# Kernel tuning notes

Measured on AMD Instinct MI355X. Metric: run time of the kernel, lower is better.

## Reference

```python
import jax, jax.numpy as jnp
import numpy as np

N = 100000
IN_F = 165
HID = 128
E = 1600000


def gcn_conv(x, W, b, src, dst, n):
    # PyG GCNConv: h = x @ W; add self-loops; symmetric norm D^-1/2 A D^-1/2; aggregate; + bias
    h = x @ W  # [n, out]
    src_sl = jnp.concatenate([src, jnp.arange(n)])
    dst_sl = jnp.concatenate([dst, jnp.arange(n)])
    deg = jax.ops.segment_sum(jnp.ones_like(src_sl, dtype=h.dtype), dst_sl, num_segments=n)
    dinv = jnp.where(deg > 0, jax.lax.rsqrt(deg), 0.0)
    norm = dinv[src_sl] * dinv[dst_sl]  # [e+n]
    msg = h[src_sl] * norm[:, None]
    out = jax.ops.segment_sum(msg, dst_sl, num_segments=n)
    return out + b


def setup_inputs() -> dict:
    key = jax.random.key(0)
    k = jax.random.split(key, 8)
    x = jax.random.normal(k[0], (N, IN_F), dtype=jnp.float32)
    edge_index = jax.random.randint(k[1], (2, E), 0, N)
    s1 = 1.0 / np.sqrt(IN_F)
    s2 = 1.0 / np.sqrt(HID)
    W1 = jax.random.uniform(k[2], (IN_F, HID), jnp.float32, -s1, s1)
    b1 = jnp.zeros((HID,), jnp.float32)
    W2 = jax.random.uniform(k[3], (HID, HID), jnp.float32, -s2, s2)
    b2 = jnp.zeros((HID,), jnp.float32)
    Wc = jax.random.uniform(k[4], (HID, 2), jnp.float32, -s2, s2)
    bc = jax.random.uniform(k[5], (2,), jnp.float32, -s2, s2)
    return {"x": x, "edge_index": edge_index, "W1": W1, "b1": b1,
            "W2": W2, "b2": b2, "Wc": Wc, "bc": bc}


def reference(x, edge_index, W1, b1, W2, b2, Wc, bc):
    src, dst = edge_index[0], edge_index[1]
    h = jax.nn.relu(gcn_conv(x, W1, b1, src, dst, N))
    # dropout inactive (eval mode)
    h = jax.nn.relu(gcn_conv(h, W2, b2, src, dst, N))
    return h @ Wc + bc
```

## Files before the change

kernel.cpp:

```cpp
#include <hip/hip_runtime.h>


typedef _Float16 half8 __attribute__((ext_vector_type(8)));
typedef float floatx4 __attribute__((ext_vector_type(4)));
typedef float f4u __attribute__((ext_vector_type(4), aligned(4)));

#define SLOT_C 64
#define BCAP 4608
#define NBKT 391
#define CHUNK 4096

__global__ __launch_bounds__(256) void multisplit_k(const int* __restrict__ src,
                                                    const int* __restrict__ dst, int e,
                                                    int* __restrict__ bcnt,
                                                    int2* __restrict__ edges2) {
  __shared__ int lhist[NBKT];
  __shared__ int lbase[NBKT];
  __shared__ int lcur[NBKT];
  int t = threadIdx.x;
  int e0 = blockIdx.x * CHUNK;
  int e1 = min(e0 + CHUNK, e);
  for (int b = t; b < NBKT; b += 256) { lhist[b] = 0; lcur[b] = 0; }
  __syncthreads();
  for (int i = e0 + t; i < e1; i += 256)
    atomicAdd(&lhist[dst[i] >> 8], 1);
  __syncthreads();
  for (int b = t; b < NBKT; b += 256) {
    int h = lhist[b];
    lbase[b] = h ? atomicAdd(&bcnt[b], h) : 0;
  }
  __syncthreads();
  for (int i = e0 + t; i < e1; i += 256) {
    int d = dst[i];
    int b = d >> 8;
    int p = lbase[b] + atomicAdd(&lcur[b], 1);
    if (p < BCAP) edges2[(size_t)b * BCAP + p] = make_int2(src[i], d);
  }
}

__global__ __launch_bounds__(256) void csr_from_bins_k(const int2* __restrict__ edges2,
                                                       const int* __restrict__ bcnt,
                                                       int* __restrict__ csr,
                                                       float* __restrict__ dinv, int n) {
  __shared__ int lcnt[256];
  int b = blockIdx.x;
  int node0 = b << 8;
  int t = threadIdx.x;
  lcnt[t] = 0;
  __syncthreads();
  int ec = min(bcnt[b], BCAP);
  const int2* ebase = edges2 + (size_t)b * BCAP;
  for (int i = t; i < ec; i += 256) {
    int2 ed = ebase[i];
    int p = atomicAdd(&lcnt[ed.y - node0], 1);
    if (p < SLOT_C - 1) csr[((size_t)ed.y << 6) + p] = ed.x;
  }
  __syncthreads();
  int node = node0 + t;
  if (node < n) {
    int c = lcnt[t];
    csr[((size_t)node << 6) + (SLOT_C - 1)] = c;
    dinv[node] = rsqrtf((float)(c + 1));
  }
}

__global__ void w_split_frag_k(const float* __restrict__ W, int K, int nslab,
                               _Float16* __restrict__ WF) {
  int idx = blockIdx.x * blockDim.x + threadIdx.x;
  if (idx >= nslab * 8192) return;
  int j = idx & 7;
  int lane = (idx >> 3) & 63;
  int p = (idx >> 9) & 1;
  int c = (idx >> 10) & 7;
  int s = idx >> 13;
  int k = (s << 5) + ((lane >> 4) << 3) + j;
  int col = (c << 4) + (lane & 15);
  float v = (k < K) ? W[(size_t)k * 128 + col] : 0.f;
  _Float16 h = (_Float16)v;
  WF[idx] = p ? (_Float16)(v - (float)h) : h;
}

template <bool AHALF, int NSLAB>
__global__ __launch_bounds__(256) void gemm_f16_k(const void* __restrict__ Av,
                                                  const _Float16* __restrict__ WF,
                                                  const float* __restrict__ rowscale,
                                                  _Float16* __restrict__ out,
                                                  int n, int K) {
  int wave = threadIdx.x >> 6, lane = threadIdx.x & 63;
  int m = lane & 15, quad = lane >> 4;
  int rowbase = blockIdx.x * 128 + wave * 32;
  int ra[2];
  ra[0] = min(rowbase + m, n - 1);
  ra[1] = min(rowbase + 16 + m, n - 1);

  floatx4 acc[2][8];
#pragma unroll
  for (int t = 0; t < 2; ++t)
#pragma unroll
    for (int c = 0; c < 8; ++c) acc[t][c] = (floatx4){0.f, 0.f, 0.f, 0.f};

  f4u xb[3][2][2];
  half8 hb[3][2];

  auto loadA = [&](int s, int b) {
    int k0 = (s << 5) + quad * 8;
#pragma unroll
    for (int t = 0; t < 2; ++t) {
      if constexpr (AHALF) {
        const _Float16* arow = (const _Float16*)Av + (size_t)ra[t] * K;
        hb[b][t] = *(const half8*)(arow + k0);
      } else {
        const float* arow = (const float*)Av + (size_t)ra[t] * K;
        if ((s << 5) + 32 <= K) {
          xb[b][t][0] = *(const f4u*)(arow + k0);
          xb[b][t][1] = *(const f4u*)(arow + k0 + 4);
        } else {
#pragma unroll
          for (int j = 0; j < 4; ++j) { int kk = k0 + j;     kk = kk < K ? kk : K - 1; xb[b][t][0][j] = arow[kk]; }
#pragma unroll
          for (int j = 0; j < 4; ++j) { int kk = k0 + 4 + j; kk = kk < K ? kk : K - 1; xb[b][t][1][j] = arow[kk]; }
        }
      }
    }
  };

  loadA(0, 0);
  if (NSLAB > 1) loadA(1, 1);

#pragma unroll
  for (int s = 0; s < NSLAB; ++s) {
    const _Float16* wbase = WF + (size_t)s * 8192;
    half8 wh[8], wl[8];
#pragma unroll
    for (int c = 0; c < 8; ++c) {
      wh[c] = *(const half8*)(wbase + c * 1024 + lane * 8);
      wl[c] = *(const half8*)(wbase + c * 1024 + 512 + lane * 8);
    }
    if (s + 2 < NSLAB) loadA(s + 2, (s + 2) % 3);

    int b = s % 3;
    half8 ah[2], al[2];
#pragma unroll
    for (int t = 0; t < 2; ++t) {
      if constexpr (AHALF) {
        ah[t] = hb[b][t];
      } else {
#pragma unroll
        for (int j = 0; j < 8; ++j) {
          float v = (j < 4) ? xb[b][t][0][j] : xb[b][t][1][j - 4];
          _Float16 hh = (_Float16)v;
          ah[t][j] = hh;
          al[t][j] = (_Float16)(v - (float)hh);
        }
      }
    }
#pragma unroll
    for (int c = 0; c < 8; ++c)
#pragma unroll
      for (int t = 0; t < 2; ++t) {
        acc[t][c] = __builtin_amdgcn_mfma_f32_16x16x32_f16(ah[t], wh[c], acc[t][c], 0, 0, 0);
        acc[t][c] = __builtin_amdgcn_mfma_f32_16x16x32_f16(ah[t], wl[c], acc[t][c], 0, 0, 0);
        if constexpr (!AHALF)
          acc[t][c] = __builtin_amdgcn_mfma_f32_16x16x32_f16(al[t], wh[c], acc[t][c], 0, 0, 0);
      }
  }

#pragma unroll
  for (int t = 0; t < 2; ++t) {
#pragma unroll
    for (int i = 0; i < 4; ++i) {
      int row = rowbase + t * 16 + quad * 4 + i;
      if (row < n) {
        float di = rowscale ? rowscale[row] : 1.0f;
#pragma unroll
        for (int c = 0; c < 8; ++c)
          out[(size_t)row * 128 + c * 16 + m] = (_Float16)(acc[t][c][i] * di);
      }
    }
  }
}

template <bool CLS>
__global__ __launch_bounds__(256) void aggregate_k(const _Float16* __restrict__ g,
                                                   const int* __restrict__ csr,
                                                   const float* __restrict__ dinv,
                                                   const float* __restrict__ bias,
                                                   const float* __restrict__ Wc,
                                                   const float* __restrict__ bc,
                                                   _Float16* __restrict__ out16,
                                                   float* __restrict__ out32, int n) {
  int wave = threadIdx.x >> 6;
  int lane = threadIdx.x & 63;
  int i = blockIdx.x * 4 + wave;
  if (i >= n) return;
  int qtr = lane >> 4;
  int l16 = lane & 15;
  int f = l16 * 8;

  int sv = csr[((size_t)i << 6) + lane];
  half8 self = *(const half8*)&g[(size_t)i * 128 + f];
  float di = dinv[i];
  float4 b0 = *(const float4*)&bias[f];
  float4 b1 = *(const float4*)&bias[f + 4];

  int deg = min(__shfl(sv, SLOT_C - 1, 64), SLOT_C - 1);

  float acc[8];
#pragma unroll
  for (int j = 0; j < 8; ++j) acc[j] = 0.f;

  auto grp = [&](int k) {
    int ee = 4 * k + qtr;
    bool valid = ee < deg;
    int ec = valid ? ee : 0;
    int srow = __shfl(sv, ec, 64);
    half8 v = *(const half8*)&g[(size_t)srow * 128 + f];
    float w = valid ? 1.f : 0.f;
#pragma unroll
    for (int j = 0; j < 8; ++j) acc[j] = fmaf(w, (float)v[j], acc[j]);
  };

  if (deg > 0) {
    if (deg <= 16) {
#pragma unroll
      for (int k = 0; k < 4; ++k) grp(k);
    } else if (deg <= 32) {
#pragma unroll
      for (int k = 0; k < 8; ++k) grp(k);
    } else {
#pragma unroll
      for (int k = 0; k < 16; ++k) grp(k);
    }
#pragma unroll
    for (int j = 0; j < 8; ++j) {
      acc[j] += __shfl_xor(acc[j], 16, 64);
      acc[j] += __shfl_xor(acc[j], 32, 64);
    }
  }

  float bv[8] = {b0.x, b0.y, b0.z, b0.w, b1.x, b1.y, b1.z, b1.w};
  float r[8];
#pragma unroll
  for (int j = 0; j < 8; ++j)
    r[j] = fmaxf((acc[j] + (float)self[j]) * di + bv[j], 0.f);

  if (!CLS) {
    if (qtr == 0) {
      half8 o;
#pragma unroll
      for (int j = 0; j < 8; ++j) o[j] = (_Float16)(r[j] * di);
      *(half8*)&out16[(size_t)i * 128 + f] = o;
    }
  } else {
    float c0v = 0.f, c1v = 0.f;
#pragma unroll
    for (int q = 0; q < 4; ++q) {
      float4 wv = *(const float4*)&Wc[f * 2 + q * 4];
      c0v += r[q * 2] * wv.x + r[q * 2 + 1] * wv.z;
      c1v += r[q * 2] * wv.y + r[q * 2 + 1] * wv.w;
    }
#pragma unroll
    for (int off = 8; off > 0; off >>= 1) {
      c0v += __shfl_down(c0v, off, 16);
      c1v += __shfl_down(c1v, off, 16);
    }
    if (lane == 0) {
      out32[(size_t)i * 2 + 0] = c0v + bc[0];
      out32[(size_t)i * 2 + 1] = c1v + bc[1];
    }
  }
}

extern "C" void kernel_launch(void* const* d_in, const int* in_sizes, int n_in,
                              void* d_out, int out_size, void* d_ws, size_t ws_size,
                              hipStream_t stream) {
  const float* x  = (const float*)d_in[0];
  const int*   ei = (const int*)d_in[1];
  const float* W1 = (const float*)d_in[2];
  const float* b1 = (const float*)d_in[3];
  const float* W2 = (const float*)d_in[4];
  const float* b2 = (const float*)d_in[5];
  const float* Wc = (const float*)d_in[6];
  const float* bc = (const float*)d_in[7];
  float* out = (float*)d_out;

  const int IN_F = 165;
  const int NS1 = 6;
  const int NS2 = 4;
  const int n = in_sizes[0] / IN_F;
  const int e = in_sizes[1] / 2;
  const int* src = ei;
  const int* dst = ei + e;

  char* ws = (char*)d_ws;
  size_t off = 0;
  auto alloc = [&](size_t bytes) -> void* {
    void* p = ws + off;
    off += (bytes + 255) & ~(size_t)255;
    return p;
  };
  _Float16* bufA = (_Float16*)alloc((size_t)n * 128 * 2);
  _Float16* bufB = (_Float16*)alloc((size_t)n * 128 * 2);
  int*   csr  = (int*)alloc((size_t)n * SLOT_C * 4);
  int2*  edges2 = (int2*)alloc((size_t)NBKT * BCAP * 8);
  int*   bcnt = (int*)alloc((size_t)NBKT * 4);
  float* dinv = (float*)alloc((size_t)n * 4);
  _Float16* wf1 = (_Float16*)alloc((size_t)NS1 * 8192 * 2);
  _Float16* wf2 = (_Float16*)alloc((size_t)NS2 * 8192 * 2);

  hipMemsetAsync(bcnt, 0, (size_t)NBKT * 4, stream);

  w_split_frag_k<<<NS1 * 32, 256, 0, stream>>>(W1, IN_F, NS1, wf1);
  w_split_frag_k<<<NS2 * 32, 256, 0, stream>>>(W2, 128, NS2, wf2);

  multisplit_k<<<(e + CHUNK - 1) / CHUNK, 256, 0, stream>>>(src, dst, e, bcnt, edges2);
  csr_from_bins_k<<<NBKT, 256, 0, stream>>>(edges2, bcnt, csr, dinv, n);

  const int gemmgrid = (n + 127) / 128;
  gemm_f16_k<false, NS1><<<gemmgrid, 256, 0, stream>>>(x, wf1, dinv, bufA, n, IN_F);
  aggregate_k<false><<<(n + 3) / 4, 256, 0, stream>>>(bufA, csr, dinv, b1, nullptr, nullptr,
                                                      bufB, nullptr, n);
  gemm_f16_k<true, NS2><<<gemmgrid, 256, 0, stream>>>(bufB, wf2, nullptr, bufA, n, 128);
  aggregate_k<true><<<(n + 3) / 4, 256, 0, stream>>>(bufA, csr, dinv, b2, Wc, bc,
                                                     nullptr, out, n);
}
```

Baseline: 342.2 us.

## Split feature matrix and CSR into halves for cache-friendly aggregation

Splits the 128-wide fp16 hidden feature buffers into two 64-column halves. Each aggregation block handles one half for four nodes, with blocks interleaved so both halves of a node group run close together, and each wave covers 8 edges per step instead of 4. This shrinks the gathered working set per pass, so the half-size feature table is more likely to stay in L2/LLC during random gathers. The CSR is split into a 31-entry primary slab plus an overflow slab, so low-degree nodes read less index data. The classifier output now takes two atomic adds per node into a zeroed output, which adds a memset, doubles the number of blocks, and needs extra shuffles.

```diff
diff --git a/kernel.cpp b/kernel.cpp
--- a/kernel.cpp
+++ b/kernel.cpp
@@ -40,7 +40,8 @@
 
 __global__ __launch_bounds__(256) void csr_from_bins_k(const int2* __restrict__ edges2,
                                                        const int* __restrict__ bcnt,
-                                                       int* __restrict__ csr,
+                                                       int* __restrict__ csrA,
+                                                       int* __restrict__ csrB,
                                                        float* __restrict__ dinv, int n) {
   __shared__ int lcnt[256];
   int b = blockIdx.x;
@@ -53,13 +54,14 @@
   for (int i = t; i < ec; i += 256) {
     int2 ed = ebase[i];
     int p = atomicAdd(&lcnt[ed.y - node0], 1);
-    if (p < SLOT_C - 1) csr[((size_t)ed.y << 6) + p] = ed.x;
+    if (p < 31) csrA[((size_t)ed.y << 5) + p] = ed.x;
+    else if (p < SLOT_C - 1) csrB[((size_t)ed.y << 5) + (p - 31)] = ed.x;
   }
   __syncthreads();
   int node = node0 + t;
   if (node < n) {
     int c = lcnt[t];
-    csr[((size_t)node << 6) + (SLOT_C - 1)] = c;
+    csrA[((size_t)node << 5) + 31] = c;
     dinv[node] = rsqrtf((float)(c + 1));
   }
 }
@@ -81,10 +83,12 @@
 }
 
 template <bool AHALF, int NSLAB>
-__global__ __launch_bounds__(256) void gemm_f16_k(const void* __restrict__ Av,
+__global__ __launch_bounds__(256) void gemm_f16_k(const void* __restrict__ A0,
+                                                  const void* __restrict__ A1,
                                                   const _Float16* __restrict__ WF,
                                                   const float* __restrict__ rowscale,
-                                                  _Float16* __restrict__ out,
+                                                  _Float16* __restrict__ out0,
+                                                  _Float16* __restrict__ out1,
                                                   int n, int K) {
   int wave = threadIdx.x >> 6, lane = threadIdx.x & 63;
   int m = lane & 15, quad = lane >> 4;
@@ -107,10 +111,10 @@
 #pragma unroll
     for (int t = 0; t < 2; ++t) {
       if constexpr (AHALF) {
-        const _Float16* arow = (const _Float16*)Av + (size_t)ra[t] * K;
-        hb[b][t] = *(const half8*)(arow + k0);
+        const _Float16* base = (const _Float16*)(((s << 5) < 64) ? A0 : A1);
+        hb[b][t] = *(const half8*)(base + (size_t)ra[t] * 64 + (k0 & 63));
       } else {
-        const float* arow = (const float*)Av + (size_t)ra[t] * K;
+        const float* arow = (const float*)A0 + (size_t)ra[t] * K;
         if ((s << 5) + 32 <= K) {
           xb[b][t][0] = *(const f4u*)(arow + k0);
           xb[b][t][1] = *(const f4u*)(arow + k0 + 4);
@@ -173,48 +177,57 @@
       if (row < n) {
         float di = rowscale ? rowscale[row] : 1.0f;
 #pragma unroll
-        for (int c = 0; c < 8; ++c)
-          out[(size_t)row * 128 + c * 16 + m] = (_Float16)(acc[t][c][i] * di);
+        for (int c = 0; c < 8; ++c) {
+          _Float16* o = (c < 4) ? out0 : out1;
+          o[(size_t)row * 64 + (c & 3) * 16 + m] = (_Float16)(acc[t][c][i] * di);
+        }
       }
     }
   }
 }
 
 template <bool CLS>
-__global__ __launch_bounds__(256) void aggregate_k(const _Float16* __restrict__ g,
-                                                   const int* __restrict__ csr,
+__global__ __launch_bounds__(256) void aggregate_k(const _Float16* __restrict__ g0,
+                                                   const _Float16* __restrict__ g1,
+                                                   const int* __restrict__ csrA,
+                                                   const int* __restrict__ csrB,
                                                    const float* __restrict__ dinv,
                                                    const float* __restrict__ bias,
                                                    const float* __restrict__ Wc,
                                                    const float* __restrict__ bc,
-                                                   _Float16* __restrict__ out16,
+                                                   _Float16* __restrict__ o0,
+                                                   _Float16* __restrict__ o1,
                                                    float* __restrict__ out32, int n) {
   int wave = threadIdx.x >> 6;
   int lane = threadIdx.x & 63;
-  int i = blockIdx.x * 4 + wave;
+  int blk = blockIdx.x;
+  int h = (blk >> 2) & 1;
+  int ng = (blk >> 3) * 4 + (blk & 3);
+  int i = ng * 4 + wave;
   if (i >= n) return;
-  int qtr = lane >> 4;
-  int l16 = lane & 15;
-  int f = l16 * 8;
-
-  int sv = csr[((size_t)i << 6) + lane];
-  half8 self = *(const half8*)&g[(size_t)i * 128 + f];
+  int g8 = lane >> 3;
+  int f = (lane & 7) * 8;
+
+  const _Float16* g = h ? g1 : g0;
+
+  int sv = csrA[((size_t)i << 5) + (lane & 31)];
+  half8 self = *(const half8*)&g[(size_t)i * 64 + f];
   float di = dinv[i];
-  float4 b0 = *(const float4*)&bias[f];
-  float4 b1 = *(const float4*)&bias[f + 4];
-
-  int deg = min(__shfl(sv, SLOT_C - 1, 64), SLOT_C - 1);
+  float4 bv0 = *(const float4*)&bias[h * 64 + f];
+  float4 bv1 = *(const float4*)&bias[h * 64 + f + 4];
+
+  int deg = min(__shfl(sv, 31, 64), SLOT_C - 1);
 
   float acc[8];
 #pragma unroll
   for (int j = 0; j < 8; ++j) acc[j] = 0.f;
 
-  auto grp = [&](int k) {
-    int ee = 4 * k + qtr;
+  auto grpS = [&](int k) {
+    int ee = 8 * k + g8;
     bool valid = ee < deg;
     int ec = valid ? ee : 0;
     int srow = __shfl(sv, ec, 64);
-    half8 v = *(const half8*)&g[(size_t)srow * 128 + f];
+    half8 v = *(const half8*)&g[(size_t)srow * 64 + f];
     float w = valid ? 1.f : 0.f;
 #pragma unroll
     for (int j = 0; j < 8; ++j) acc[j] = fmaf(w, (float)v[j], acc[j]);
@@ -222,51 +235,63 @@
 
   if (deg > 0) {
     if (deg <= 16) {
-#pragma unroll
-      for (int k = 0; k < 4; ++k) grp(k);
-    } else if (deg <= 32) {
-#pragma unroll
-      for (int k = 0; k < 8; ++k) grp(k);
+      grpS(0); grpS(1);
+    } else if (deg <= 31) {
+#pragma unroll
+      for (int k = 0; k < 4; ++k) grpS(k);
     } else {
-#pragma unroll
-      for (int k = 0; k < 16; ++k) grp(k);
+      int sv2 = csrB[((size_t)i << 5) + (lane & 31)];
+#pragma unroll
+      for (int k = 0; k < 8; ++k) {
+        int ee = 8 * k + g8;
+        bool valid = ee < deg;
+        int ec = valid ? ee : 0;
+        int sA = __shfl(sv, ec < 31 ? ec : 0, 64);
+        int sB = __shfl(sv2, ec >= 31 ? ec - 31 : 0, 64);
+        int srow = (ec < 31) ? sA : sB;
+        half8 v = *(const half8*)&g[(size_t)srow * 64 + f];
+        float w = valid ? 1.f : 0.f;
+#pragma unroll
+        for (int j = 0; j < 8; ++j) acc[j] = fmaf(w, (float)v[j], acc[j]);
+      }
     }
 #pragma unroll
     for (int j = 0; j < 8; ++j) {
+      acc[j] += __shfl_xor(acc[j], 8, 64);
       acc[j] += __shfl_xor(acc[j], 16, 64);
       acc[j] += __shfl_xor(acc[j], 32, 64);
     }
   }
 
-  float bv[8] = {b0.x, b0.y, b0.z, b0.w, b1.x, b1.y, b1.z, b1.w};
+  float bv[8] = {bv0.x, bv0.y, bv0.z, bv0.w, bv1.x, bv1.y, bv1.z, bv1.w};
   float r[8];
 #pragma unroll
   for (int j = 0; j < 8; ++j)
     r[j] = fmaxf((acc[j] + (float)self[j]) * di + bv[j], 0.f);
 
   if (!CLS) {
-    if (qtr == 0) {
+    if (g8 == 0) {
       half8 o;
 #pragma unroll
       for (int j = 0; j < 8; ++j) o[j] = (_Float16)(r[j] * di);
-      *(half8*)&out16[(size_t)i * 128 + f] = o;
+      *(half8*)&((h ? o1 : o0)[(size_t)i * 64 + f]) = o;
     }
   } else {
     float c0v = 0.f, c1v = 0.f;
 #pragma unroll
     for (int q = 0; q < 4; ++q) {
-      float4 wv = *(const float4*)&Wc[f * 2 + q * 4];
+      float4 wv = *(const float4*)&Wc[(h * 64 + f) * 2 + q * 4];
       c0v += r[q * 2] * wv.x + r[q * 2 + 1] * wv.z;
       c1v += r[q * 2] * wv.y + r[q * 2 + 1] * wv.w;
     }
 #pragma unroll
-    for (int off = 8; off > 0; off >>= 1) {
-      c0v += __shfl_down(c0v, off, 16);
-      c1v += __shfl_down(c1v, off, 16);
+    for (int off = 4; off > 0; off >>= 1) {
+      c0v += __shfl_down(c0v, off, 8);
+      c1v += __shfl_down(c1v, off, 8);
     }
     if (lane == 0) {
-      out32[(size_t)i * 2 + 0] = c0v + bc[0];
-      out32[(size_t)i * 2 + 1] = c1v + bc[1];
+      atomicAdd(&out32[(size_t)i * 2 + 0], h == 0 ? c0v + bc[0] : c0v);
+      atomicAdd(&out32[(size_t)i * 2 + 1], h == 0 ? c1v + bc[1] : c1v);
     }
   }
 }
@@ -299,9 +324,12 @@
     off += (bytes + 255) & ~(size_t)255;
     return p;
   };
-  _Float16* bufA = (_Float16*)alloc((size_t)n * 128 * 2);
-  _Float16* bufB = (_Float16*)alloc((size_t)n * 128 * 2);
-  int*   csr  = (int*)alloc((size_t)n * SLOT_C * 4);
+  _Float16* bufA0 = (_Float16*)alloc((size_t)n * 64 * 2);
+  _Float16* bufA1 = (_Float16*)alloc((size_t)n * 64 * 2);
+  _Float16* bufB0 = (_Float16*)alloc((size_t)n * 64 * 2);
+  _Float16* bufB1 = (_Float16*)alloc((size_t)n * 64 * 2);
+  int*   csrA = (int*)alloc((size_t)n * 32 * 4);
+  int*   csrB = (int*)alloc((size_t)n * 32 * 4);
   int2*  edges2 = (int2*)alloc((size_t)NBKT * BCAP * 8);
   int*   bcnt = (int*)alloc((size_t)NBKT * 4);
   float* dinv = (float*)alloc((size_t)n * 4);
@@ -309,18 +337,24 @@
   _Float16* wf2 = (_Float16*)alloc((size_t)NS2 * 8192 * 2);
 
   hipMemsetAsync(bcnt, 0, (size_t)NBKT * 4, stream);
+  hipMemsetAsync(out, 0, (size_t)n * 2 * sizeof(float), stream);
 
   w_split_frag_k<<<NS1 * 32, 256, 0, stream>>>(W1, IN_F, NS1, wf1);
   w_split_frag_k<<<NS2 * 32, 256, 0, stream>>>(W2, 128, NS2, wf2);
 
   multisplit_k<<<(e + CHUNK - 1) / CHUNK, 256, 0, stream>>>(src, dst, e, bcnt, edges2);
-  csr_from_bins_k<<<NBKT, 256, 0, stream>>>(edges2, bcnt, csr, dinv, n);
+  csr_from_bins_k<<<NBKT, 256, 0, stream>>>(edges2, bcnt, csrA, csrB, dinv, n);
 
   const int gemmgrid = (n + 127) / 128;
-  gemm_f16_k<false, NS1><<<gemmgrid, 256, 0, stream>>>(x, wf1, dinv, bufA, n, IN_F);
-  aggregate_k<false><<<(n + 3) / 4, 256, 0, stream>>>(bufA, csr, dinv, b1, nullptr, nullptr,
-                                                      bufB, nullptr, n);
-  gemm_f16_k<true, NS2><<<gemmgrid, 256, 0, stream>>>(bufB, wf2, nullptr, bufA, n, 128);
-  aggregate_k<true><<<(n + 3) / 4, 256, 0, stream>>>(bufA, csr, dinv, b2, Wc, bc,
-                                                     nullptr, out, n);
-}
+  const int G = (n + 3) / 4;
+  const int Gp = (G + 3) & ~3;
+  const int agrid = 2 * Gp;
+  gemm_f16_k<false, NS1><<<gemmgrid, 256, 0, stream>>>(x, nullptr, wf1, dinv,
+                                                       bufA0, bufA1, n, IN_F);
+  aggregate_k<false><<<agrid, 256, 0, stream>>>(bufA0, bufA1, csrA, csrB, dinv, b1,
+                                                nullptr, nullptr, bufB0, bufB1, nullptr, n);
+  gemm_f16_k<true, NS2><<<gemmgrid, 256, 0, stream>>>(bufB0, bufB1, wf2, nullptr,
+                                                      bufA0, bufA1, n, 128);
+  aggregate_k<true><<<agrid, 256, 0, stream>>>(bufA0, bufA1, csrA, csrB, dinv, b2,
+                                               Wc, bc, nullptr, nullptr, out, n);
+}
```

Result: slower. 403.1 us (+17.8%).

## Replace global-atomic bucket binning with per-chunk local sort and offset table

Applied to the files above, without the earlier changes.

The edge binning step now sorts each 4096-edge chunk locally by destination bucket using a shared-memory histogram and wave prefix scan. It writes the chunk in place and records per-chunk bucket start offsets as ushort, instead of reserving slots in global buckets with atomics on a shared counter array. The CSR build kernel then walks every chunk's segment for its bucket using the offset table. This removes the global atomics, the fixed BCAP bucket capacity and its overflow truncation, and the memset. In exchange, each CSR block reads 391 small scattered segments, which gives poorly coalesced, short loops per chunk.

```diff
diff --git a/kernel.cpp b/kernel.cpp
--- a/kernel.cpp
+++ b/kernel.cpp
@@ -6,54 +6,95 @@
 typedef float f4u __attribute__((ext_vector_type(4), aligned(4)));
 
 #define SLOT_C 64
-#define BCAP 4608
 #define NBKT 391
 #define CHUNK 4096
-
-__global__ __launch_bounds__(256) void multisplit_k(const int* __restrict__ src,
+#define GSTRIDE (NBKT + 1)
+
+__global__ __launch_bounds__(256) void sort_chunk_k(const int* __restrict__ src,
                                                     const int* __restrict__ dst, int e,
-                                                    int* __restrict__ bcnt,
-                                                    int2* __restrict__ edges2) {
+                                                    int2* __restrict__ sorted,
+                                                    unsigned short* __restrict__ gstart) {
   __shared__ int lhist[NBKT];
-  __shared__ int lbase[NBKT];
+  __shared__ int lstart[NBKT];
   __shared__ int lcur[NBKT];
+  __shared__ int lsegtot[8];
   int t = threadIdx.x;
   int e0 = blockIdx.x * CHUNK;
   int e1 = min(e0 + CHUNK, e);
+  int cnt = e1 - e0;
   for (int b = t; b < NBKT; b += 256) { lhist[b] = 0; lcur[b] = 0; }
   __syncthreads();
   for (int i = e0 + t; i < e1; i += 256)
     atomicAdd(&lhist[dst[i] >> 8], 1);
   __syncthreads();
+  int wave = t >> 6, lane = t & 63;
+  for (int seg = wave; seg < 7; seg += 4) {
+    int b = seg * 64 + lane;
+    int v = (b < NBKT) ? lhist[b] : 0;
+#pragma unroll
+    for (int off = 1; off < 64; off <<= 1) {
+      int u = __shfl_up(v, off, 64);
+      if (lane >= off) v += u;
+    }
+    if (b < NBKT) lstart[b] = v;
+    if (lane == 63) lsegtot[seg] = v;
+  }
+  __syncthreads();
+  if (wave == 0) {
+    int v = (lane < 7) ? lsegtot[lane] : 0;
+#pragma unroll
+    for (int off = 1; off < 8; off <<= 1) {
+      int u = __shfl_up(v, off, 64);
+      if (lane >= off) v += u;
+    }
+    if (lane < 7) lsegtot[lane] = v;
+  }
+  __syncthreads();
   for (int b = t; b < NBKT; b += 256) {
-    int h = lhist[b];
-    lbase[b] = h ? atomicAdd(&bcnt[b], h) : 0;
-  }
+    int s = lstart[b] - lhist[b] + ((b >= 64) ? lsegtot[(b >> 6) - 1] : 0);
+    lstart[b] = s;
+    gstart[(size_t)blockIdx.x * GSTRIDE + b] = (unsigned short)s;
+  }
+  if (t == 0) gstart[(size_t)blockIdx.x * GSTRIDE + NBKT] = (unsigned short)cnt;
   __syncthreads();
   for (int i = e0 + t; i < e1; i += 256) {
     int d = dst[i];
     int b = d >> 8;
-    int p = lbase[b] + atomicAdd(&lcur[b], 1);
-    if (p < BCAP) edges2[(size_t)b * BCAP + p] = make_int2(src[i], d);
-  }
-}
-
-__global__ __launch_bounds__(256) void csr_from_bins_k(const int2* __restrict__ edges2,
-                                                       const int* __restrict__ bcnt,
-                                                       int* __restrict__ csr,
-                                                       float* __restrict__ dinv, int n) {
+    int p = lstart[b] + atomicAdd(&lcur[b], 1);
+    sorted[(size_t)blockIdx.x * CHUNK + p] = make_int2(src[i], d);
+  }
+}
+
+__global__ __launch_bounds__(256) void csr_from_sorted_k(const int2* __restrict__ sorted,
+                                                         const unsigned short* __restrict__ gstart,
+                                                         int nb, int* __restrict__ csr,
+                                                         float* __restrict__ dinv, int n) {
   __shared__ int lcnt[256];
   int b = blockIdx.x;
   int node0 = b << 8;
   int t = threadIdx.x;
   lcnt[t] = 0;
   __syncthreads();
-  int ec = min(bcnt[b], BCAP);
-  const int2* ebase = edges2 + (size_t)b * BCAP;
-  for (int i = t; i < ec; i += 256) {
-    int2 ed = ebase[i];
-    int p = atomicAdd(&lcnt[ed.y - node0], 1);
-    if (p < SLOT_C - 1) csr[((size_t)ed.y << 6) + p] = ed.x;
+  int Q = t >> 4;
+  int l16 = t & 15;
+  int s0 = 0, s1 = 0;
+  if (Q < nb) {
+    s0 = gstart[(size_t)Q * GSTRIDE + b];
+    s1 = gstart[(size_t)Q * GSTRIDE + b + 1];
+  }
+  for (int B = Q; B < nb; B += 16) {
+    int Bn = B + 16;
+    int n0 = 0, n1 = 0;
+    if (Bn < nb) {
+      n0 = gstart[(size_t)Bn * GSTRIDE + b];
+      n1 = gstart[(size_t)Bn * GSTRIDE + b + 1];
+    }
+    for (int jj = l16; jj < s1 - s0; jj += 16) {
+      int2 ed = sorted[(size_t)B * CHUNK + s0 + jj];
+      int p = atomicAdd(&lcnt[ed.y - node0], 1);
+      if (p < SLOT_C - 1) csr[((size_t)ed.y << 6) + p] = ed.x;
+    }
+    s0 = n0; s1 = n1;
   }
   __syncthreads();
   int node = node0 + t;
@@ -291,6 +332,7 @@
   const int e = in_sizes[1] / 2;
   const int* src = ei;
   const int* dst = ei + e;
+  const int NB = (e + CHUNK - 1) / CHUNK;
 
   char* ws = (char*)d_ws;
   size_t off = 0;
@@ -302,19 +344,17 @@
   _Float16* bufA = (_Float16*)alloc((size_t)n * 128 * 2);
   _Float16* bufB = (_Float16*)alloc((size_t)n * 128 * 2);
   int*   csr  = (int*)alloc((size_t)n * SLOT_C * 4);
-  int2*  edges2 = (int2*)alloc((size_t)NBKT * BCAP * 8);
-  int*   bcnt = (int*)alloc((size_t)NBKT * 4);
+  int2*  sorted = (int2*)alloc((size_t)NB * CHUNK * 8);
+  unsigned short* gstart = (unsigned short*)alloc((size_t)NB * GSTRIDE * 2);
   float* dinv = (float*)alloc((size_t)n * 4);
   _Float16* wf1 = (_Float16*)alloc((size_t)NS1 * 8192 * 2);
   _Float16* wf2 = (_Float16*)alloc((size_t)NS2 * 8192 * 2);
 
-  hipMemsetAsync(bcnt, 0, (size_t)NBKT * 4, stream);
-
   w_split_frag_k<<<NS1 * 32, 256, 0, stream>>>(W1, IN_F, NS1, wf1);
   w_split_frag_k<<<NS2 * 32, 256, 0, stream>>>(W2, 128, NS2, wf2);
 
-  multisplit_k<<<(e + CHUNK - 1) / CHUNK, 256, 0, stream>>>(src, dst, e, bcnt, edges2);
-  csr_from_bins_k<<<NBKT, 256, 0, stream>>>(edges2, bcnt, csr, dinv, n);
+  sort_chunk_k<<<NB, 256, 0, stream>>>(src, dst, e, sorted, gstart);
+  csr_from_sorted_k<<<NBKT, 256, 0, stream>>>(sorted, gstart, NB, csr, dinv, n);
 
   const int gemmgrid = (n + 127) / 128;
   gemm_f16_k<false, NS1><<<gemmgrid, 256, 0, stream>>>(x, wf1, dinv, bufA, n, IN_F);
```

New measurement: 347.4 us. Within noise of the previous version (+1.5%).

## Fuse layer-1 aggregation with layer-2 GEMM through shared memory

Applied to the files above, without the earlier changes.

Replaces the separate layer-1 aggregate kernel and layer-2 GEMM with one kernel. Each block gathers neighbour features for 128 nodes, applies bias, ReLU and degree scaling, stages the rows in LDS, then runs the MFMA GEMM against W2 directly. This drops one kernel launch and the global write and re-read of the intermediate hidden matrix. In exchange, each wave processes 32 nodes serially with neighbour loads that use only one quarter of the lanes per group, and the large LDS footprint may lower occupancy.

```diff
diff --git a/kernel.cpp b/kernel.cpp
--- a/kernel.cpp
+++ b/kernel.cpp
@@ -9,6 +9,7 @@
 #define BCAP 4608
 #define NBKT 391
 #define CHUNK 4096
+#define LROW 136
 
 __global__ __launch_bounds__(256) void multisplit_k(const int* __restrict__ src,
                                                     const int* __restrict__ dst, int e,
@@ -175,6 +176,111 @@
 #pragma unroll
         for (int c = 0; c < 8; ++c)
           out[(size_t)row * 128 + c * 16 + m] = (_Float16)(acc[t][c][i] * di);
+      }
+    }
+  }
+}
+
+__global__ __launch_bounds__(256) void agg_gemm2_k(const _Float16* __restrict__ g,
+                                                   const int* __restrict__ csr,
+                                                   const float* __restrict__ dinv,
+                                                   const float* __restrict__ bias,
+                                                   const _Float16* __restrict__ WF,
+                                                   _Float16* __restrict__ out, int n) {
+  __shared__ _Float16 hlds[128 * LROW];
+  int w = threadIdx.x >> 6, lane = threadIdx.x & 63;
+  int m = lane & 15, quad = lane >> 4;
+  int qtr = quad;
+  int f = m * 8;
+  int base = blockIdx.x * 128 + w * 32;
+
+  float4 b0 = *(const float4*)&bias[f];
+  float4 b1v = *(const float4*)&bias[f + 4];
+  float bv[8] = {b0.x, b0.y, b0.z, b0.w, b1v.x, b1v.y, b1v.z, b1v.w};
+  float dv = dinv[min(base + (lane & 31), n - 1)];
+
+  int i0 = min(base, n - 1);
+  int sv = csr[((size_t)i0 << 6) + lane];
+  half8 self = *(const half8*)&g[(size_t)i0 * 128 + f];
+  for (int nl = 0; nl < 32; ++nl) {
+    int svn = sv; half8 selfn = self;
+    if (nl < 31) {
+      int in_ = min(base + nl + 1, n - 1);
+      svn = csr[((size_t)in_ << 6) + lane];
+      selfn = *(const half8*)&g[(size_t)in_ * 128 + f];
+    }
+    int deg = min(__shfl(sv, SLOT_C - 1, 64), SLOT_C - 1);
+
+    float acc[8];
+#pragma unroll
+    for (int j = 0; j < 8; ++j) acc[j] = 0.f;
+
+    auto grp = [&](int k) {
+      int ee = 4 * k + qtr;
+      bool valid = ee < deg;
+      int ec = valid ? ee : 0;
+      int srow = __shfl(sv, ec, 64);
+      half8 v = *(const half8*)&g[(size_t)srow * 128 + f];
+      float wt = valid ? 1.f : 0.f;
+#pragma unroll
+      for (int j = 0; j < 8; ++j) acc[j] = fmaf(wt, (float)v[j], acc[j]);
+    };
+
+    if (deg > 0) {
+      if (deg <= 16) {
+#pragma unroll
+        for (int k = 0; k < 4; ++k) grp(k);
+      } else if (deg <= 32) {
+#pragma unroll
+        for (int k = 0; k < 8; ++k) grp(k);
+      } else {
+#pragma unroll
+        for (int k = 0; k < 16; ++k) grp(k);
+      }
+#pragma unroll
+      for (int j = 0; j < 8; ++j) {
+        acc[j] += __shfl_xor(acc[j], 16, 64);
+        acc[j] += __shfl_xor(acc[j], 32, 64);
+      }
+    }
+
+    float di = __shfl(dv, nl, 64);
+    if (qtr == 0) {
+      half8 o;
+#pragma unroll
+      for (int j = 0; j < 8; ++j)
+        o[j] = (_Float16)(fmaxf((acc[j] + (float)self[j]) * di + bv[j], 0.f) * di);
+      *(half8*)&hlds[(size_t)(w * 32 + nl) * LROW + f] = o;
+    }
+    sv = svn; self = selfn;
+  }
+
+  __syncthreads();
+
+#pragma unroll
+  for (int t = 0; t < 2; ++t) {
+    floatx4 acc2[8];
+#pragma unroll
+    for (int c = 0; c < 8; ++c) acc2[c] = (floatx4){0.f, 0.f, 0.f, 0.f};
+#pragma unroll
+    for (int s = 0; s < 4; ++s) {
+      half8 ah = *(const half8*)&hlds[(size_t)(w * 32 + t * 16 + m) * LROW + s * 32 + quad * 8];
+      const _Float16* wbase = WF + (size_t)s * 8192;
+#pragma unroll
+      for (int c = 0; c < 8; ++c) {
+        half8 wh = *(const half8*)(wbase + c * 1024 + lane * 8);
+        half8 wl = *(const half8*)(wbase + c * 1024 + 512 + lane * 8);
+        acc2[c] = __builtin_amdgcn_mfma_f32_16x16x32_f16(ah, wh, acc2[c], 0, 0, 0);
+        acc2[c] = __builtin_amdgcn_mfma_f32_16x16x32_f16(ah, wl, acc2[c], 0, 0, 0);
+      }
+    }
+#pragma unroll
+    for (int i = 0; i < 4; ++i) {
+      int row = blockIdx.x * 128 + w * 32 + t * 16 + quad * 4 + i;
+      if (row < n) {
+#pragma unroll
+        for (int c = 0; c < 8; ++c)
+          out[(size_t)row * 128 + c * 16 + m] = (_Float16)acc2[c][i];
       }
     }
   }
@@ -318,9 +424,7 @@
 
   const int gemmgrid = (n + 127) / 128;
   gemm_f16_k<false, NS1><<<gemmgrid, 256, 0, stream>>>(x, wf1, dinv, bufA, n, IN_F);
-  aggregate_k<false><<<(n + 3) / 4, 256, 0, stream>>>(bufA, csr, dinv, b1, nullptr, nullptr,
-                                                      bufB, nullptr, n);
-  gemm_f16_k<true, NS2><<<gemmgrid, 256, 0, stream>>>(bufB, wf2, nullptr, bufA, n, 128);
-  aggregate_k<true><<<(n + 3) / 4, 256, 0, stream>>>(bufA, csr, dinv, b2, Wc, bc,
+  agg_gemm2_k<<<gemmgrid, 256, 0, stream>>>(bufA, csr, dinv, b1, wf2, bufB, n);
+  aggregate_k<true><<<(n + 3) / 4, 256, 0, stream>>>(bufB, csr, dinv, b2, Wc, bc,
                                                      nullptr, out, n);
 }
```

Result: slower. 377.1 us (+10.2%).
